# Optimization experiments

Measured on AMD Instinct MI355X. Metric: run time of the kernel, lower is better.

## Reference

```python
import jax, jax.numpy as jnp
import numpy as np

N = 50000      # nodes
DEG = 16       # avg random degree (self-loops added on top)
IN = 256       # in_dim
HID = 32       # num_hidden per head
H = 4          # heads for hidden layers
C = 64         # num_classes (output layer has 1 head of size C)
STEPS = 10     # label_prop_steps
SLOPE = 0.2    # negative_slope


def _glorot(k, shape):
    fan = shape[0] + int(np.prod(shape[1:]))
    return jax.random.normal(k, shape, jnp.float32) * np.sqrt(2.0 / fan)


def setup_inputs() -> dict:
    key = jax.random.key(0)
    ks = jax.random.split(key, 14)
    E0 = N * DEG
    loop = jnp.arange(N, dtype=jnp.int32)
    src = jnp.concatenate([jax.random.randint(ks[0], (E0,), 0, N, jnp.int32), loop])
    dst = jnp.concatenate([jax.random.randint(ks[1], (E0,), 0, N, jnp.int32), loop])
    feat = jax.random.normal(ks[2], (N, IN), jnp.float32)
    return {
        "feat": feat, "src": src, "dst": dst,
        # layer 0: in=256 -> [4 heads, 32]
        "W0": _glorot(ks[3], (IN, H, HID)), "al0": _glorot(ks[4], (H, HID)), "ar0": _glorot(ks[5], (H, HID)),
        # layer 1: in=128 -> [4 heads, 32]
        "W1": _glorot(ks[6], (H * HID, H, HID)), "al1": _glorot(ks[7], (H, HID)), "ar1": _glorot(ks[8], (H, HID)),
        # output layer: in=128 -> [1 head, 64]
        "W2": _glorot(ks[9], (H * HID, 1, C)), "al2": _glorot(ks[10], (1, C)), "ar2": _glorot(ks[11], (1, C)),
        # weighted-pooling layer (num_classes -> num_classes, no activation)
        "Wp": _glorot(ks[12], (C, C)), "bp": jnp.zeros((C,), jnp.float32),
    }


def gat_layer(x, src, dst, W, al, ar):
    """GAT conv: returns (out [N,H,D], alpha [E,H])."""
    n = x.shape[0]
    h = jnp.einsum('ni,ihd->nhd', x, W)                    # [N,H,D]
    el = jnp.sum(h * al, axis=-1)                          # [N,H]
    er = jnp.sum(h * ar, axis=-1)                          # [N,H]
    e = el[src] + er[dst]                                  # [E,H]
    e = jnp.where(e > 0, e, SLOPE * e)                     # LeakyReLU
    m = jax.ops.segment_max(e, dst, num_segments=n)        # edge softmax over incoming edges
    p = jnp.exp(e - m[dst])
    s = jax.ops.segment_sum(p, dst, num_segments=n)
    alpha = p / (s[dst] + 1e-9)                            # [E,H]
    out = jax.ops.segment_sum(h[src] * alpha[:, :, None], dst, num_segments=n)
    return out, alpha


def reference(feat, src, dst, W0, al0, ar0, W1, al1, ar1, W2, al2, ar2, Wp, bp):
    # GAT trunk: hidden layers flatten heads + ELU, output layer means heads.
    h, a0 = gat_layer(feat, src, dst, W0, al0, ar0)
    h = jax.nn.elu(h).reshape(N, H * HID)
    h, a1 = gat_layer(h, src, dst, W1, al1, ar1)
    h = jax.nn.elu(h).reshape(N, H * HID)
    out, a2 = gat_layer(h, src, dst, W2, al2, ar2)
    logits = out.mean(axis=1)                              # [N,C]

    # mean attention over heads per layer, then over layers; detached in original
    w = jax.lax.stop_gradient(
        (a0.mean(axis=1) + a1.mean(axis=1) + a2.mean(axis=1)) / 3.0)  # [E]

    # iterative label propagation via weighted pooling + linear (num_classes->num_classes)
    pseudo = jax.nn.softmax(logits, axis=1)
    for _ in range(STEPS):
        agg = jax.ops.segment_sum(w[:, None] * pseudo[src], dst, num_segments=N)  # [N,C]
        logits = agg @ Wp + bp
        pseudo = jax.nn.softmax(logits, axis=1)
    return jnp.log(pseudo)
```

## Files before the change

kernel.cpp:

```cpp
#include <hip/hip_runtime.h>
#include <math.h>

typedef _Float16 half_t;
typedef __attribute__((ext_vector_type(2))) _Float16 half2t;
typedef __attribute__((ext_vector_type(8))) _Float16 half8;
typedef __attribute__((ext_vector_type(4))) float f32x4;

__device__ __forceinline__ half2t u2h2(unsigned u){ half2t h; __builtin_memcpy(&h, &u, 4); return h; }
__device__ __forceinline__ unsigned h22u(half2t h){ unsigned u; __builtin_memcpy(&u, &h, 4); return u; }
__device__ __forceinline__ unsigned packh2(float a, float b){
  half2t h; h[0] = (_Float16)a; h[1] = (_Float16)b; return h22u(h);
}

__device__ __forceinline__ float wsumf(float v){
#pragma unroll
  for (int off = 1; off < 64; off <<= 1) v += __shfl_xor(v, off, 64);
  return v;
}


__global__ void k_zerob(int* __restrict__ a, int n){
  int i = blockIdx.x * blockDim.x + threadIdx.x;
  if (i < n) a[i] = 0;
}

__global__ __launch_bounds__(256) void kb_hist(
    const int* __restrict__ dst, int* __restrict__ bsum, int E, int NB)
{
  __shared__ int cnt[512];
  int t = threadIdx.x;
  int e00 = blockIdx.x * 2048;
  for (int i = t; i < NB; i += 256) cnt[i] = 0;
  __syncthreads();
#pragma unroll
  for (int k = 0; k < 8; k++){
    int e = e00 + 256 * k + t;
    if (e < E) atomicAdd(&cnt[dst[e] >> 7], 1);
  }
  __syncthreads();
  for (int i = t; i < NB; i += 256){
    int c = cnt[i];
    if (c) atomicAdd(&bsum[i], c);
  }
}

__global__ __launch_bounds__(512) void kb_scan(
    const int* __restrict__ bsum, int* __restrict__ bb, int* __restrict__ gcur,
    int E, int NB)
{
  __shared__ int sh[512];
  int t = threadIdx.x;
  int v = (t < NB) ? bsum[t] : 0;
  sh[t] = v; __syncthreads();
  for (int s = 1; s < 512; s <<= 1){
    int u = (t >= s) ? sh[t - s] : 0;
    __syncthreads();
    sh[t] += u;
    __syncthreads();
  }
  if (t < NB){
    int ex = sh[t] - v;
    bb[t] = ex; gcur[t] = ex;
  }
  if (t == 0) bb[NB] = E;
}

__global__ __launch_bounds__(256) void kb_scat(
    const int* __restrict__ src, const int* __restrict__ dst,
    int* __restrict__ gcur, int2* __restrict__ ebuf, int E, int NB)
{
  __shared__ int cnt[512], base[512];
  int t = threadIdx.x;
  int e00 = blockIdx.x * 2048;
  for (int i = t; i < NB; i += 256) cnt[i] = 0;
  __syncthreads();
  int bk[8], sv[8], dv[8];
#pragma unroll
  for (int k = 0; k < 8; k++){
    int e = e00 + 256 * k + t;
    if (e < E){
      dv[k] = dst[e]; sv[k] = src[e];
      bk[k] = dv[k] >> 7;
      atomicAdd(&cnt[bk[k]], 1);
    } else bk[k] = -1;
  }
  __syncthreads();
  for (int i = t; i < NB; i += 256){
    int c = cnt[i];
    base[i] = c ? atomicAdd(&gcur[i], c) : 0;
    cnt[i] = 0;
  }
  __syncthreads();
#pragma unroll
  for (int k = 0; k < 8; k++){
    if (bk[k] >= 0){
      int pos = base[bk[k]] + atomicAdd(&cnt[bk[k]], 1);
      ebuf[pos] = make_int2(sv[k], dv[k]);
    }
  }
}

__global__ __launch_bounds__(256) void kb_sort(
    const int2* __restrict__ ebuf, const int* __restrict__ bb,
    int* __restrict__ ptre, int* __restrict__ srcs, int N, int E)
{
  __shared__ int cnt[128], off[128];
  int b = blockIdx.x, t = threadIdx.x;
  int e0 = bb[b], e1 = bb[b + 1];
  int nn0 = b << 7;
  if (t < 128) cnt[t] = 0;
  __syncthreads();
  for (int e = e0 + t; e < e1; e += 256)
    atomicAdd(&cnt[ebuf[e].y & 127], 1);
  __syncthreads();
  if (t < 128) off[t] = cnt[t];
  __syncthreads();
  for (int s = 1; s < 128; s <<= 1){
    int v = (t < 128 && t >= s) ? off[t - s] : 0;
    __syncthreads();
    if (t < 128) off[t] += v;
    __syncthreads();
  }
  if (t < 128){
    int ex = off[t] - cnt[t];
    off[t] = ex;
    int node = nn0 + t;
    if (node < N) ptre[node] = e0 + ex;
    cnt[t] = 0;
  }
  if (b == (int)gridDim.x - 1 && t == 0) ptre[N] = E;
  __syncthreads();
  for (int e = e0 + t; e < e1; e += 256){
    int2 ed = ebuf[e];
    int lo = ed.y & 127;
    int pos = atomicAdd(&cnt[lo], 1);
    srcs[e0 + off[lo] + pos] = ed.x;
  }
}

__global__ void k_cvtw(const float* __restrict__ W0, const float* __restrict__ W1,
                       const float* __restrict__ W2, const float* __restrict__ Wp,
                       half_t* __restrict__ T0, half_t* __restrict__ T1,
                       half_t* __restrict__ T2, half_t* __restrict__ Tp){
  int i = blockIdx.x * 256 + threadIdx.x;
  const float* src; half_t* dst; int NN, KK, idx;
  if (i < 32768){ src = W0; dst = T0; NN = 128; KK = 256; idx = i; }
  else if (i < 49152){ src = W1; dst = T1; NN = 128; KK = 128; idx = i - 32768; }
  else if (i < 57344){ src = W2; dst = T2; NN = 64; KK = 128; idx = i - 49152; }
  else { src = Wp; dst = Tp; NN = 64; KK = 64; idx = i - 57344; }
  int nn = idx / KK, kk = idx - nn * KK;
  dst[idx] = (_Float16)src[(size_t)kk * NN + nn];
}

template<int NC, int NH, bool XF32>
__global__ __launch_bounds__(256) void k_gemm_m(
    const void* __restrict__ Xv, const half_t* __restrict__ Wt,
    const float* __restrict__ al, const float* __restrict__ ar,
    half_t* __restrict__ Yh, float* __restrict__ el, float* __restrict__ er,
    int n, int KD)
{
  constexpr int CT = NC / 16;
  __shared__ __align__(16) half_t xs[64 * 72];
  __shared__ __align__(16) half_t ws[NC * 72];
  int tid = threadIdx.x;
  int w = tid >> 6, lane = tid & 63;
  int m = lane & 15, q = lane >> 4;
  int n0 = blockIdx.x * 64;
  f32x4 acc[CT];
#pragma unroll
  for (int ct = 0; ct < CT; ct++) acc[ct] = (f32x4){0.f, 0.f, 0.f, 0.f};

  for (int kc = 0; kc < KD; kc += 64){
    if (XF32){
      const float* X = (const float*)Xv;
#pragma unroll
      for (int s = tid; s < 512; s += 256){
        int r = s >> 3, off = (s & 7) * 8;
        int gr = min(n0 + r, n - 1);
        const float4* g = (const float4*)(X + (size_t)gr * KD + kc + off);
        float4 v0 = g[0], v1 = g[1];
        uint4 pk = make_uint4(packh2(v0.x, v0.y), packh2(v0.z, v0.w),
                              packh2(v1.x, v1.y), packh2(v1.z, v1.w));
        *(uint4*)&xs[r * 72 + off] = pk;
      }
    } else {
      const half_t* X = (const half_t*)Xv;
#pragma unroll
      for (int s = tid; s < 512; s += 256){
        int r = s >> 3, off = (s & 7) * 8;
        int gr = min(n0 + r, n - 1);
        *(uint4*)&xs[r * 72 + off] = *(const uint4*)(X + (size_t)gr * KD + kc + off);
      }
    }
#pragma unroll
    for (int s = tid; s < NC * 8; s += 256){
      int r = s >> 3, off = (s & 7) * 8;
      *(uint4*)&ws[r * 72 + off] = *(const uint4*)(Wt + (size_t)r * KD + kc + off);
    }
    __syncthreads();
    half8 a0 = *(const half8*)&xs[(16 * w + m) * 72 + q * 8];
    half8 a1 = *(const half8*)&xs[(16 * w + m) * 72 + 32 + q * 8];
#pragma unroll
    for (int ct = 0; ct < CT; ct++){
      half8 b0 = *(const half8*)&ws[(16 * ct + m) * 72 + q * 8];
      half8 b1 = *(const half8*)&ws[(16 * ct + m) * 72 + 32 + q * 8];
      acc[ct] = __builtin_amdgcn_mfma_f32_16x16x32_f16(a0, b0, acc[ct], 0, 0, 0);
      acc[ct] = __builtin_amdgcn_mfma_f32_16x16x32_f16(a1, b1, acc[ct], 0, 0, 0);
    }
    __syncthreads();
  }

#pragma unroll
  for (int j = 0; j < 4; j++){
    int gr = n0 + 16 * w + q * 4 + j;
    if (gr < n){
#pragma unroll
      for (int ct = 0; ct < CT; ct++)
        Yh[(size_t)gr * NC + 16 * ct + m] = (_Float16)acc[ct][j];
    }
  }
  float alv[CT], arv[CT];
#pragma unroll
  for (int ct = 0; ct < CT; ct++){ alv[ct] = al[16 * ct + m]; arv[ct] = ar[16 * ct + m]; }
#pragma unroll
  for (int j = 0; j < 4; j++){
    int gr = n0 + 16 * w + q * 4 + j;
    float ev[NH], rv[NH];
    if (NH == 4){
#pragma unroll
      for (int hh = 0; hh < 4; hh++){
        ev[hh] = acc[2 * hh][j] * alv[2 * hh] + acc[2 * hh + 1][j] * alv[2 * hh + 1];
        rv[hh] = acc[2 * hh][j] * arv[2 * hh] + acc[2 * hh + 1][j] * arv[2 * hh + 1];
      }
    } else {
      ev[0] = 0.f; rv[0] = 0.f;
#pragma unroll
      for (int ct = 0; ct < CT; ct++){
        ev[0] += acc[ct][j] * alv[ct];
        rv[0] += acc[ct][j] * arv[ct];
      }
    }
#pragma unroll
    for (int off = 1; off < 16; off <<= 1){
#pragma unroll
      for (int hh = 0; hh < NH; hh++){
        ev[hh] += __shfl_xor(ev[hh], off, 64);
        rv[hh] += __shfl_xor(rv[hh], off, 64);
      }
    }
    if (m == 0 && gr < n){
#pragma unroll
      for (int hh = 0; hh < NH; hh++){
        el[(size_t)gr * NH + hh] = ev[hh];
        er[(size_t)gr * NH + hh] = rv[hh];
      }
    }
  }
}

template<int HNUM, int MDIM, int EPI>
__global__ __launch_bounds__(64) void k_edge(
    const int* __restrict__ ptre, const int* __restrict__ srcs,
    const char* __restrict__ hb, const float* __restrict__ el,
    const float* __restrict__ er, half_t* __restrict__ outx,
    unsigned char* __restrict__ outu, float* __restrict__ wE,
    int2* __restrict__ epk, int init_w, int n)
{
  constexpr int LL = MDIM / 8;
  constexpr int EP = 64 / LL;
  constexpr int RB = MDIM * 2;
  constexpr int HID = MDIM / HNUM;
  __shared__ unsigned au[HNUM][264];
  __shared__ int sids[256];
  int node = blockIdx.x;
  if (node >= n) return;
  int lane = threadIdx.x;
  int base = ptre[node], deg = ptre[node + 1] - base;

  float erv[HNUM];
  if (HNUM == 4){
    float4 t = *reinterpret_cast<const float4*>(er + node * 4);
    erv[0] = t.x; erv[1] = t.y; erv[2] = t.z; erv[3] = t.w;
  } else erv[0] = er[node];

  int l = lane % LL, g = lane / LL;
  int hidx = (8 * l) / HID;
  half2t acc2[4];
#pragma unroll
  for (int k = 0; k < 4; k++) acc2[k] = (half2t){(_Float16)0.f, (_Float16)0.f};

  if (deg <= 64){
    float pv[HNUM], sm[HNUM];
#pragma unroll
    for (int h = 0; h < HNUM; h++){ pv[h] = 0.f; sm[h] = 0.f; }
    int s = -1;
    if (lane < deg){
      s = srcs[base + lane];
      sids[lane] = s * RB;
      float e[HNUM];
      if (HNUM == 4){
        float4 t = *reinterpret_cast<const float4*>(el + s * 4);
        e[0] = t.x; e[1] = t.y; e[2] = t.z; e[3] = t.w;
      } else e[0] = el[s];
#pragma unroll
      for (int h = 0; h < HNUM; h++){
        float v = e[h] + erv[h];
        v = v > 0.f ? v : 0.2f * v;
        pv[h] = __expf(v);
        sm[h] = pv[h];
      }
    }
    float inv[HNUM];
#pragma unroll
    for (int h = 0; h < HNUM; h++) inv[h] = 1.f / (wsumf(sm[h]) + 1e-9f);
    if (lane < deg){
      float wsum = 0.f;
#pragma unroll
      for (int h = 0; h < HNUM; h++){
        float a = pv[h] * inv[h];
        wsum += a;
        au[h][lane] = packh2(a, a);
      }
      wsum *= (1.f / (3.f * HNUM));
      int eidx = base + lane;
      if (EPI == 1){
        float wtot = (wE[eidx] + wsum) * (1.f / 255.f);
        epk[eidx] = make_int2(s * 64, __float_as_int(wtot));
      } else {
        wE[eidx] = init_w ? wsum : (wE[eidx] + wsum);
      }
    }
    __syncthreads();
    for (int j0 = 0; j0 < deg; j0 += EP){
      int j = j0 + g;
      if (j < deg){
        half2t a2 = u2h2(au[hidx][j]);
        uint4 v = *(const uint4*)(hb + (unsigned)sids[j] + 16 * l);
        acc2[0] += a2 * u2h2(v.x);
        acc2[1] += a2 * u2h2(v.y);
        acc2[2] += a2 * u2h2(v.z);
        acc2[3] += a2 * u2h2(v.w);
      }
    }
  } else {
    float sm[HNUM];
#pragma unroll
    for (int h = 0; h < HNUM; h++) sm[h] = 0.f;
    for (int i = lane; i < deg; i += 64){
      int s = srcs[base + i];
      if (i < 256) sids[i] = s * RB;
      float e[HNUM];
      if (HNUM == 4){
        float4 t = *reinterpret_cast<const float4*>(el + s * 4);
        e[0] = t.x; e[1] = t.y; e[2] = t.z; e[3] = t.w;
      } else e[0] = el[s];
#pragma unroll
      for (int h = 0; h < HNUM; h++){
        float v = e[h] + erv[h];
        v = v > 0.f ? v : 0.2f * v;
        float p = __expf(v);
        sm[h] += p;
        if (i < 256) au[h][i] = __float_as_uint(p);
      }
    }
    float inv[HNUM];
#pragma unroll
    for (int h = 0; h < HNUM; h++) inv[h] = 1.f / (wsumf(sm[h]) + 1e-9f);

    for (int c0 = 0; c0 < deg; c0 += 256){
      int cnt = min(256, deg - c0);
      for (int i = lane; i < cnt; i += 64){
        float p[HNUM]; int soff;
        if (c0 == 0){
          soff = sids[i];
#pragma unroll
          for (int h = 0; h < HNUM; h++) p[h] = __uint_as_float(au[h][i]);
        } else {
          int s = srcs[base + c0 + i];
          soff = s * RB;
          sids[i] = soff;
          float e[HNUM];
          if (HNUM == 4){
            float4 t = *reinterpret_cast<const float4*>(el + s * 4);
            e[0] = t.x; e[1] = t.y; e[2] = t.z; e[3] = t.w;
          } else e[0] = el[s];
#pragma unroll
          for (int h = 0; h < HNUM; h++){
            float v = e[h] + erv[h];
            v = v > 0.f ? v : 0.2f * v;
            p[h] = __expf(v);
          }
        }
        float wsum = 0.f;
#pragma unroll
        for (int h = 0; h < HNUM; h++){
          float a = p[h] * inv[h];
          wsum += a;
          au[h][i] = packh2(a, a);
        }
        wsum *= (1.f / (3.f * HNUM));
        int eidx = base + c0 + i;
        if (EPI == 1){
          float wtot = (wE[eidx] + wsum) * (1.f / 255.f);
          epk[eidx] = make_int2(soff >> 1, __float_as_int(wtot));
        } else {
          wE[eidx] = init_w ? wsum : (wE[eidx] + wsum);
        }
      }
      __syncthreads();
      for (int j0 = 0; j0 < cnt; j0 += EP){
        int j = j0 + g;
        if (j < cnt){
          half2t a2 = u2h2(au[hidx][j]);
          uint4 v = *(const uint4*)(hb + (unsigned)sids[j] + 16 * l);
          acc2[0] += a2 * u2h2(v.x);
          acc2[1] += a2 * u2h2(v.y);
          acc2[2] += a2 * u2h2(v.z);
          acc2[3] += a2 * u2h2(v.w);
        }
      }
      __syncthreads();
    }
  }

#pragma unroll
  for (int off = LL; off < 64; off <<= 1)
#pragma unroll
    for (int k = 0; k < 4; k++)
      acc2[k] += u2h2((unsigned)__shfl_xor((int)h22u(acc2[k]), off, 64));

  float o[8];
#pragma unroll
  for (int k = 0; k < 4; k++){
    o[2 * k] = (float)acc2[k][0];
    o[2 * k + 1] = (float)acc2[k][1];
  }
  if (EPI == 0){
    if (g == 0){
#pragma unroll
      for (int d = 0; d < 8; d++) o[d] = o[d] > 0.f ? o[d] : expm1f(o[d]);
      uint4 pk = make_uint4(packh2(o[0], o[1]), packh2(o[2], o[3]),
                            packh2(o[4], o[5]), packh2(o[6], o[7]));
      reinterpret_cast<uint4*>(outx + (size_t)node * MDIM)[l] = pk;
    }
  } else {
    float m8 = o[0];
#pragma unroll
    for (int d = 1; d < 8; d++) m8 = fmaxf(m8, o[d]);
#pragma unroll
    for (int off = 1; off < 8; off <<= 1) m8 = fmaxf(m8, __shfl_xor(m8, off, 64));
    float p[8], s8 = 0.f;
#pragma unroll
    for (int d = 0; d < 8; d++){ p[d] = __expf(o[d] - m8); s8 += p[d]; }
#pragma unroll
    for (int off = 1; off < 8; off <<= 1) s8 += __shfl_xor(s8, off, 64);
    float is = 255.f / s8;
    if (g == 0){
      unsigned b0 = 0, b1 = 0;
#pragma unroll
      for (int d = 0; d < 4; d++) b0 |= ((unsigned)(int)(p[d] * is + 0.5f)) << (8 * d);
#pragma unroll
      for (int d = 0; d < 4; d++) b1 |= ((unsigned)(int)(p[4 + d] * is + 0.5f)) << (8 * d);
      *reinterpret_cast<uint2*>(outu + (size_t)node * 64 + 8 * l) = make_uint2(b0, b1);
    }
  }
}

template<int FINAL>
__global__ __launch_bounds__(256) void k_lpu(
    const int* __restrict__ ptre, const int2* __restrict__ epk,
    const unsigned char* __restrict__ pb, const half_t* __restrict__ Tp,
    const float* __restrict__ bp, unsigned char* __restrict__ outu,
    float* __restrict__ outf, int n)
{
  __shared__ __align__(16) half_t xs[64 * 72];
  __shared__ __align__(16) half_t ws[64 * 72];
  __shared__ float bsh[64];
  int tid = threadIdx.x;
  int w = tid >> 6, lane = tid & 63;
  int n0 = blockIdx.x * 64;
#pragma unroll
  for (int s = tid; s < 512; s += 256){
    int r = s >> 3, off = (s & 7) * 8;
    *(uint4*)&ws[r * 72 + off] = *(const uint4*)(Tp + r * 64 + off);
  }
  if (tid < 64) bsh[tid] = bp[tid];

  int grp = tid >> 2;
  int l4 = tid & 3;
  int node = n0 + grp;
  float acc[16];
#pragma unroll
  for (int c = 0; c < 16; c++) acc[c] = 0.f;

  auto accum = [&](uint4 v, float wv){
#pragma unroll
    for (int b = 0; b < 4; b++){
      unsigned u = (&v.x)[b];
      acc[4 * b + 0] += wv * (float)(u & 0xffu);
      acc[4 * b + 1] += wv * (float)((u >> 8) & 0xffu);
      acc[4 * b + 2] += wv * (float)((u >> 16) & 0xffu);
      acc[4 * b + 3] += wv * (float)((u >> 24) & 0xffu);
    }
  };

  if (node < n){
    int j = ptre[node], endd = ptre[node + 1];
    int bo = 16 * l4;
    while (j + 4 <= endd){
      int2 e0 = epk[j], e1 = epk[j + 1], e2 = epk[j + 2], e3 = epk[j + 3];
      uint4 v0 = *(const uint4*)(pb + (unsigned)e0.x + bo);
      uint4 v1 = *(const uint4*)(pb + (unsigned)e1.x + bo);
      uint4 v2 = *(const uint4*)(pb + (unsigned)e2.x + bo);
      uint4 v3 = *(const uint4*)(pb + (unsigned)e3.x + bo);
      accum(v0, __int_as_float(e0.y));
      accum(v1, __int_as_float(e1.y));
      accum(v2, __int_as_float(e2.y));
      accum(v3, __int_as_float(e3.y));
      j += 4;
    }
    while (j < endd){
      int2 ep = epk[j];
      uint4 v = *(const uint4*)(pb + (unsigned)ep.x + bo);
      accum(v, __int_as_float(ep.y));
      j++;
    }
  }
  {
    half2t hp[8];
#pragma unroll
    for (int c = 0; c < 8; c++){
      hp[c][0] = (_Float16)acc[2 * c]; hp[c][1] = (_Float16)acc[2 * c + 1];
    }
    *(uint4*)&xs[grp * 72 + 16 * l4]     = *(uint4*)&hp[0];
    *(uint4*)&xs[grp * 72 + 16 * l4 + 8] = *(uint4*)&hp[4];
  }
  __syncthreads();

  int m = lane & 15, q = lane >> 4;
  f32x4 macc[4];
#pragma unroll
  for (int ct = 0; ct < 4; ct++) macc[ct] = (f32x4){0.f, 0.f, 0.f, 0.f};
  half8 a0 = *(const half8*)&xs[(16 * w + m) * 72 + q * 8];
  half8 a1 = *(const half8*)&xs[(16 * w + m) * 72 + 32 + q * 8];
#pragma unroll
  for (int ct = 0; ct < 4; ct++){
    half8 b0 = *(const half8*)&ws[(16 * ct + m) * 72 + q * 8];
    half8 b1 = *(const half8*)&ws[(16 * ct + m) * 72 + 32 + q * 8];
    macc[ct] = __builtin_amdgcn_mfma_f32_16x16x32_f16(a0, b0, macc[ct], 0, 0, 0);
    macc[ct] = __builtin_amdgcn_mfma_f32_16x16x32_f16(a1, b1, macc[ct], 0, 0, 0);
  }

#pragma unroll
  for (int j = 0; j < 4; j++){
    int gr = n0 + 16 * w + q * 4 + j;
    float v[4]; float mx = -INFINITY;
#pragma unroll
    for (int ct = 0; ct < 4; ct++){
      v[ct] = macc[ct][j] + bsh[16 * ct + m];
      mx = fmaxf(mx, v[ct]);
    }
#pragma unroll
    for (int off = 1; off < 16; off <<= 1) mx = fmaxf(mx, __shfl_xor(mx, off, 64));
    float p[4], s = 0.f;
#pragma unroll
    for (int ct = 0; ct < 4; ct++){ p[ct] = __expf(v[ct] - mx); s += p[ct]; }
#pragma unroll
    for (int off = 1; off < 16; off <<= 1) s += __shfl_xor(s, off, 64);
    if (gr < n){
      if (FINAL){
        float ls = __logf(s);
#pragma unroll
        for (int ct = 0; ct < 4; ct++)
          outf[(size_t)gr * 64 + 16 * ct + m] = v[ct] - mx - ls;
      } else {
        float is = 255.f / s;
#pragma unroll
        for (int ct = 0; ct < 4; ct++)
          outu[(size_t)gr * 64 + 16 * ct + m] =
              (unsigned char)(int)(p[ct] * is + 0.5f);
      }
    }
  }
}

extern "C" void kernel_launch(void* const* d_in, const int* in_sizes, int n_in,
                              void* d_out, int out_size, void* d_ws, size_t ws_size,
                              hipStream_t stream) {
  const float* feat = (const float*)d_in[0];
  const int*   src  = (const int*)d_in[1];
  const int*   dst  = (const int*)d_in[2];
  const float* W0   = (const float*)d_in[3];
  const float* al0  = (const float*)d_in[4];
  const float* ar0  = (const float*)d_in[5];
  const float* W1   = (const float*)d_in[6];
  const float* al1  = (const float*)d_in[7];
  const float* ar1  = (const float*)d_in[8];
  const float* W2   = (const float*)d_in[9];
  const float* al2  = (const float*)d_in[10];
  const float* ar2  = (const float*)d_in[11];
  const float* Wp   = (const float*)d_in[12];
  const float* bp   = (const float*)d_in[13];
  float* out = (float*)d_out;

  const int N = in_sizes[0] / 256;
  const int E = in_sizes[1];
  const int NB = (N + 127) / 128;

  char* p = (char*)d_ws;
  auto carve = [&](size_t bytes) -> void* {
    void* r = (void*)p;
    p += (bytes + 255) & ~(size_t)255;
    return r;
  };
  int*   ptr_i = (int*)carve((size_t)(N + 1) * 4);
  int*   bsum  = (int*)carve((size_t)NB * 4);
  int*   bb    = (int*)carve((size_t)(NB + 1) * 4);
  int*   gcur  = (int*)carve((size_t)NB * 4);
  int*   srcs  = (int*)carve((size_t)E * 4);
  float* wE    = (float*)carve((size_t)E * 4);
  int2*  epk   = (int2*)carve((size_t)E * 8);
  half_t* hb   = (half_t*)carve((size_t)N * 128 * 2);
  half_t* xb   = (half_t*)carve((size_t)N * 128 * 2);
  float* el    = (float*)carve((size_t)N * 4 * 4);
  float* er    = (float*)carve((size_t)N * 4 * 4);
  unsigned char* pbA = (unsigned char*)carve((size_t)N * 64);
  unsigned char* pbB = (unsigned char*)carve((size_t)N * 64);
  half_t* T0   = (half_t*)carve(32768 * 2);
  half_t* T1   = (half_t*)carve(16384 * 2);
  half_t* T2   = (half_t*)carve(8192 * 2);
  half_t* Tp   = (half_t*)carve(4096 * 2);
  int2* ebuf = epk;
  (void)ws_size; (void)n_in; (void)out_size;

  const int EB = (E + 2047) / 2048;
  k_zerob<<<(NB + 255) / 256, 256, 0, stream>>>(bsum, NB);
  kb_hist<<<EB, 256, 0, stream>>>(dst, bsum, E, NB);
  kb_scan<<<1, 512, 0, stream>>>(bsum, bb, gcur, E, NB);
  kb_scat<<<EB, 256, 0, stream>>>(src, dst, gcur, ebuf, E, NB);
  kb_sort<<<NB, 256, 0, stream>>>(ebuf, bb, ptr_i, srcs, N, E);
  k_cvtw<<<240, 256, 0, stream>>>(W0, W1, W2, Wp, T0, T1, T2, Tp);

  const int GG = (N + 63) / 64;
  k_gemm_m<128, 4, true><<<GG, 256, 0, stream>>>(feat, T0, al0, ar0, hb, el, er, N, 256);
  k_edge<4, 128, 0><<<N, 64, 0, stream>>>(ptr_i, srcs, (const char*)hb, el, er,
                                          xb, nullptr, wE, nullptr, 1, N);
  k_gemm_m<128, 4, false><<<GG, 256, 0, stream>>>(xb, T1, al1, ar1, hb, el, er, N, 128);
  k_edge<4, 128, 0><<<N, 64, 0, stream>>>(ptr_i, srcs, (const char*)hb, el, er,
                                          xb, nullptr, wE, nullptr, 0, N);
  k_gemm_m<64, 1, false><<<GG, 256, 0, stream>>>(xb, T2, al2, ar2, hb, el, er, N, 128);
  k_edge<1, 64, 1><<<N, 64, 0, stream>>>(ptr_i, srcs, (const char*)hb, el, er,
                                         nullptr, pbA, wE, epk, 0, N);

  unsigned char* cur = pbA; unsigned char* nxt = pbB;
  for (int st = 0; st < 10; st++){
    if (st == 9)
      k_lpu<1><<<GG, 256, 0, stream>>>(ptr_i, epk, cur, Tp, bp, nullptr, out, N);
    else
      k_lpu<0><<<GG, 256, 0, stream>>>(ptr_i, epk, cur, Tp, bp, nxt, nullptr, N);
    unsigned char* t = cur; cur = nxt; nxt = t;
  }
}
```

Measured before the change: 480.6 us.

## Pack four nodes per edge block via shuffles; split label-prop edges across two lanes

The edge-attention kernel now runs four nodes per 256-thread block, one wavefront each. Source offsets and attention weights are broadcast with wavefront shuffles instead of shared memory and block barriers, and high-degree nodes recompute exponentials per 64-edge chunk. The label-propagation kernel doubles its threads to 512 so each node's edge list is split between two lane groups, which are then combined with a shuffle before the MFMA step. The aim is less launch overhead, fewer syncs and more memory-level parallelism on the gathers, at the cost of recomputing exponentials for large degrees and leaving half the waves idle during the matmul.

```diff
diff --git a/kernel.cpp b/kernel.cpp
--- a/kernel.cpp
+++ b/kernel.cpp
@@ -17,7 +17,6 @@
   for (int off = 1; off < 64; off <<= 1) v += __shfl_xor(v, off, 64);
   return v;
 }
-
 
 __global__ void k_zerob(int* __restrict__ a, int n){
   int i = blockIdx.x * blockDim.x + threadIdx.x;
@@ -259,7 +258,7 @@
 }
 
 template<int HNUM, int MDIM, int EPI>
-__global__ __launch_bounds__(64) void k_edge(
+__global__ __launch_bounds__(256) void k_edge(
     const int* __restrict__ ptre, const int* __restrict__ srcs,
     const char* __restrict__ hb, const float* __restrict__ el,
     const float* __restrict__ er, half_t* __restrict__ outx,
@@ -269,12 +268,9 @@
   constexpr int LL = MDIM / 8;
   constexpr int EP = 64 / LL;
   constexpr int RB = MDIM * 2;
-  constexpr int HID = MDIM / HNUM;
-  __shared__ unsigned au[HNUM][264];
-  __shared__ int sids[256];
-  int node = blockIdx.x;
+  int node = blockIdx.x * 4 + (threadIdx.x >> 6);
   if (node >= n) return;
-  int lane = threadIdx.x;
+  int lane = threadIdx.x & 63;
   int base = ptre[node], deg = ptre[node + 1] - base;
 
   float erv[HNUM];
@@ -284,19 +280,19 @@
   } else erv[0] = er[node];
 
   int l = lane % LL, g = lane / LL;
-  int hidx = (8 * l) / HID;
+  int hidx = l >> 2;
+  int bo = 16 * l;
   half2t acc2[4];
 #pragma unroll
   for (int k = 0; k < 4; k++) acc2[k] = (half2t){(_Float16)0.f, (_Float16)0.f};
 
-  if (deg <= 64){
-    float pv[HNUM], sm[HNUM];
-#pragma unroll
-    for (int h = 0; h < HNUM; h++){ pv[h] = 0.f; sm[h] = 0.f; }
-    int s = -1;
-    if (lane < deg){
-      s = srcs[base + lane];
-      sids[lane] = s * RB;
+  float inv[HNUM];
+  if (deg > 64){
+    float sm[HNUM];
+#pragma unroll
+    for (int h = 0; h < HNUM; h++) sm[h] = 0.f;
+    for (int i = lane; i < deg; i += 64){
+      int s = srcs[base + i];
       float e[HNUM];
       if (HNUM == 4){
         float4 t = *reinterpret_cast<const float4*>(el + s * 4);
@@ -306,121 +302,76 @@
       for (int h = 0; h < HNUM; h++){
         float v = e[h] + erv[h];
         v = v > 0.f ? v : 0.2f * v;
+        sm[h] += __expf(v);
+      }
+    }
+#pragma unroll
+    for (int h = 0; h < HNUM; h++) inv[h] = 1.f / (wsumf(sm[h]) + 1e-9f);
+  }
+
+  for (int c0 = 0; c0 < deg; c0 += 64){
+    int cnt = min(64, deg - c0);
+    int soff = 0; unsigned pa = 0, pb2 = 0;
+    float pv[HNUM];
+    int s = 0;
+    if (lane < cnt){
+      s = srcs[base + c0 + lane];
+      float e[HNUM];
+      if (HNUM == 4){
+        float4 t = *reinterpret_cast<const float4*>(el + s * 4);
+        e[0] = t.x; e[1] = t.y; e[2] = t.z; e[3] = t.w;
+      } else e[0] = el[s];
+#pragma unroll
+      for (int h = 0; h < HNUM; h++){
+        float v = e[h] + erv[h];
+        v = v > 0.f ? v : 0.2f * v;
         pv[h] = __expf(v);
-        sm[h] = pv[h];
-      }
-    }
-    float inv[HNUM];
-#pragma unroll
-    for (int h = 0; h < HNUM; h++) inv[h] = 1.f / (wsumf(sm[h]) + 1e-9f);
-    if (lane < deg){
-      float wsum = 0.f;
-#pragma unroll
-      for (int h = 0; h < HNUM; h++){
-        float a = pv[h] * inv[h];
-        wsum += a;
-        au[h][lane] = packh2(a, a);
-      }
+      }
+    } else {
+#pragma unroll
+      for (int h = 0; h < HNUM; h++) pv[h] = 0.f;
+    }
+    if (deg <= 64){
+#pragma unroll
+      for (int h = 0; h < HNUM; h++) inv[h] = 1.f / (wsumf(pv[h]) + 1e-9f);
+    }
+    if (lane < cnt){
+      float a[HNUM], wsum = 0.f;
+#pragma unroll
+      for (int h = 0; h < HNUM; h++){ a[h] = pv[h] * inv[h]; wsum += a[h]; }
+      if (HNUM == 4){ pa = packh2(a[0], a[1]); pb2 = packh2(a[2], a[3]); }
+      else pa = packh2(a[0], a[0]);
       wsum *= (1.f / (3.f * HNUM));
-      int eidx = base + lane;
+      int eidx = base + c0 + lane;
       if (EPI == 1){
         float wtot = (wE[eidx] + wsum) * (1.f / 255.f);
         epk[eidx] = make_int2(s * 64, __float_as_int(wtot));
       } else {
         wE[eidx] = init_w ? wsum : (wE[eidx] + wsum);
       }
-    }
-    __syncthreads();
-    for (int j0 = 0; j0 < deg; j0 += EP){
+      soff = s * RB;
+    }
+    for (int j0 = 0; j0 < cnt; j0 += EP){
       int j = j0 + g;
-      if (j < deg){
-        half2t a2 = u2h2(au[hidx][j]);
-        uint4 v = *(const uint4*)(hb + (unsigned)sids[j] + 16 * l);
+      int so = __shfl(soff, j, 64);
+      unsigned paj = (unsigned)__shfl((int)pa, j, 64);
+      unsigned pbj = 0;
+      if (HNUM == 4) pbj = (unsigned)__shfl((int)pb2, j, 64);
+      if (j < cnt){
+        unsigned a2u;
+        if (HNUM == 4){
+          unsigned sel = (hidx < 2) ? paj : pbj;
+          unsigned hb16 = (hidx & 1) ? (sel >> 16) : (sel & 0xffffu);
+          a2u = hb16 | (hb16 << 16);
+        } else a2u = paj;
+        half2t a2 = u2h2(a2u);
+        uint4 v = *(const uint4*)(hb + (unsigned)so + bo);
         acc2[0] += a2 * u2h2(v.x);
         acc2[1] += a2 * u2h2(v.y);
         acc2[2] += a2 * u2h2(v.z);
         acc2[3] += a2 * u2h2(v.w);
       }
     }
-  } else {
-    float sm[HNUM];
-#pragma unroll
-    for (int h = 0; h < HNUM; h++) sm[h] = 0.f;
-    for (int i = lane; i < deg; i += 64){
-      int s = srcs[base + i];
-      if (i < 256) sids[i] = s * RB;
-      float e[HNUM];
-      if (HNUM == 4){
-        float4 t = *reinterpret_cast<const float4*>(el + s * 4);
-        e[0] = t.x; e[1] = t.y; e[2] = t.z; e[3] = t.w;
-      } else e[0] = el[s];
-#pragma unroll
-      for (int h = 0; h < HNUM; h++){
-        float v = e[h] + erv[h];
-        v = v > 0.f ? v : 0.2f * v;
-        float p = __expf(v);
-        sm[h] += p;
-        if (i < 256) au[h][i] = __float_as_uint(p);
-      }
-    }
-    float inv[HNUM];
-#pragma unroll
-    for (int h = 0; h < HNUM; h++) inv[h] = 1.f / (wsumf(sm[h]) + 1e-9f);
-
-    for (int c0 = 0; c0 < deg; c0 += 256){
-      int cnt = min(256, deg - c0);
-      for (int i = lane; i < cnt; i += 64){
-        float p[HNUM]; int soff;
-        if (c0 == 0){
-          soff = sids[i];
-#pragma unroll
-          for (int h = 0; h < HNUM; h++) p[h] = __uint_as_float(au[h][i]);
-        } else {
-          int s = srcs[base + c0 + i];
-          soff = s * RB;
-          sids[i] = soff;
-          float e[HNUM];
-          if (HNUM == 4){
-            float4 t = *reinterpret_cast<const float4*>(el + s * 4);
-            e[0] = t.x; e[1] = t.y; e[2] = t.z; e[3] = t.w;
-          } else e[0] = el[s];
-#pragma unroll
-          for (int h = 0; h < HNUM; h++){
-            float v = e[h] + erv[h];
-            v = v > 0.f ? v : 0.2f * v;
-            p[h] = __expf(v);
-          }
-        }
-        float wsum = 0.f;
-#pragma unroll
-        for (int h = 0; h < HNUM; h++){
-          float a = p[h] * inv[h];
-          wsum += a;
-          au[h][i] = packh2(a, a);
-        }
-        wsum *= (1.f / (3.f * HNUM));
-        int eidx = base + c0 + i;
-        if (EPI == 1){
-          float wtot = (wE[eidx] + wsum) * (1.f / 255.f);
-          epk[eidx] = make_int2(soff >> 1, __float_as_int(wtot));
-        } else {
-          wE[eidx] = init_w ? wsum : (wE[eidx] + wsum);
-        }
-      }
-      __syncthreads();
-      for (int j0 = 0; j0 < cnt; j0 += EP){
-        int j = j0 + g;
-        if (j < cnt){
-          half2t a2 = u2h2(au[hidx][j]);
-          uint4 v = *(const uint4*)(hb + (unsigned)sids[j] + 16 * l);
-          acc2[0] += a2 * u2h2(v.x);
-          acc2[1] += a2 * u2h2(v.y);
-          acc2[2] += a2 * u2h2(v.z);
-          acc2[3] += a2 * u2h2(v.w);
-        }
-      }
-      __syncthreads();
-    }
   }
 
 #pragma unroll
@@ -467,7 +418,7 @@
 }
 
 template<int FINAL>
-__global__ __launch_bounds__(256) void k_lpu(
+__global__ __launch_bounds__(512) void k_lpu(
     const int* __restrict__ ptre, const int2* __restrict__ epk,
     const unsigned char* __restrict__ pb, const half_t* __restrict__ Tp,
     const float* __restrict__ bp, unsigned char* __restrict__ outu,
@@ -479,15 +430,16 @@
   int tid = threadIdx.x;
   int w = tid >> 6, lane = tid & 63;
   int n0 = blockIdx.x * 64;
-#pragma unroll
-  for (int s = tid; s < 512; s += 256){
-    int r = s >> 3, off = (s & 7) * 8;
+  {
+    int r = tid >> 3, off = (tid & 7) * 8;
     *(uint4*)&ws[r * 72 + off] = *(const uint4*)(Tp + r * 64 + off);
   }
   if (tid < 64) bsh[tid] = bp[tid];
 
-  int grp = tid >> 2;
-  int l4 = tid & 3;
+  int grp = tid >> 3;
+  int l8 = tid & 7;
+  int st = l8 >> 2, li = l8 & 3;
+  int bo = 16 * li;
   int node = n0 + grp;
   float acc[16];
 #pragma unroll
@@ -505,37 +457,36 @@
   };
 
   if (node < n){
-    int j = ptre[node], endd = ptre[node + 1];
-    int bo = 16 * l4;
-    while (j + 4 <= endd){
-      int2 e0 = epk[j], e1 = epk[j + 1], e2 = epk[j + 2], e3 = epk[j + 3];
-      uint4 v0 = *(const uint4*)(pb + (unsigned)e0.x + bo);
-      uint4 v1 = *(const uint4*)(pb + (unsigned)e1.x + bo);
-      uint4 v2 = *(const uint4*)(pb + (unsigned)e2.x + bo);
-      uint4 v3 = *(const uint4*)(pb + (unsigned)e3.x + bo);
-      accum(v0, __int_as_float(e0.y));
-      accum(v1, __int_as_float(e1.y));
-      accum(v2, __int_as_float(e2.y));
-      accum(v3, __int_as_float(e3.y));
-      j += 4;
-    }
-    while (j < endd){
-      int2 ep = epk[j];
-      uint4 v = *(const uint4*)(pb + (unsigned)ep.x + bo);
-      accum(v, __int_as_float(ep.y));
-      j++;
-    }
-  }
-  {
+    int base = ptre[node], endd = ptre[node + 1];
+    for (int j0 = base + 4 * st; j0 < endd; j0 += 8){
+      int2 ee[4]; float wv[4];
+#pragma unroll
+      for (int k = 0; k < 4; k++){
+        int j = j0 + k;
+        ee[k] = epk[min(j, endd - 1)];
+        wv[k] = (j < endd) ? __int_as_float(ee[k].y) : 0.f;
+      }
+      uint4 vv[4];
+#pragma unroll
+      for (int k = 0; k < 4; k++)
+        vv[k] = *(const uint4*)(pb + (unsigned)ee[k].x + bo);
+#pragma unroll
+      for (int k = 0; k < 4; k++) accum(vv[k], wv[k]);
+    }
+  }
+#pragma unroll
+  for (int c = 0; c < 16; c++) acc[c] += __shfl_xor(acc[c], 4, 64);
+  if (st == 0){
     half2t hp[8];
 #pragma unroll
     for (int c = 0; c < 8; c++){
       hp[c][0] = (_Float16)acc[2 * c]; hp[c][1] = (_Float16)acc[2 * c + 1];
     }
-    *(uint4*)&xs[grp * 72 + 16 * l4]     = *(uint4*)&hp[0];
-    *(uint4*)&xs[grp * 72 + 16 * l4 + 8] = *(uint4*)&hp[4];
-  }
-  __syncthreads();
+    *(uint4*)&xs[grp * 72 + 16 * li]     = *(uint4*)&hp[0];
+    *(uint4*)&xs[grp * 72 + 16 * li + 8] = *(uint4*)&hp[4];
+  }
+  __syncthreads();
+  if (w >= 4) return;
 
   int m = lane & 15, q = lane >> 4;
   f32x4 macc[4];
@@ -642,22 +593,23 @@
   k_cvtw<<<240, 256, 0, stream>>>(W0, W1, W2, Wp, T0, T1, T2, Tp);
 
   const int GG = (N + 63) / 64;
+  const int GE = (N + 3) / 4;
   k_gemm_m<128, 4, true><<<GG, 256, 0, stream>>>(feat, T0, al0, ar0, hb, el, er, N, 256);
-  k_edge<4, 128, 0><<<N, 64, 0, stream>>>(ptr_i, srcs, (const char*)hb, el, er,
-                                          xb, nullptr, wE, nullptr, 1, N);
+  k_edge<4, 128, 0><<<GE, 256, 0, stream>>>(ptr_i, srcs, (const char*)hb, el, er,
+                                            xb, nullptr, wE, nullptr, 1, N);
   k_gemm_m<128, 4, false><<<GG, 256, 0, stream>>>(xb, T1, al1, ar1, hb, el, er, N, 128);
-  k_edge<4, 128, 0><<<N, 64, 0, stream>>>(ptr_i, srcs, (const char*)hb, el, er,
-                                          xb, nullptr, wE, nullptr, 0, N);
+  k_edge<4, 128, 0><<<GE, 256, 0, stream>>>(ptr_i, srcs, (const char*)hb, el, er,
+                                            xb, nullptr, wE, nullptr, 0, N);
   k_gemm_m<64, 1, false><<<GG, 256, 0, stream>>>(xb, T2, al2, ar2, hb, el, er, N, 128);
-  k_edge<1, 64, 1><<<N, 64, 0, stream>>>(ptr_i, srcs, (const char*)hb, el, er,
-                                         nullptr, pbA, wE, epk, 0, N);
+  k_edge<1, 64, 1><<<GE, 256, 0, stream>>>(ptr_i, srcs, (const char*)hb, el, er,
+                                           nullptr, pbA, wE, epk, 0, N);
 
   unsigned char* cur = pbA; unsigned char* nxt = pbB;
   for (int st = 0; st < 10; st++){
     if (st == 9)
-      k_lpu<1><<<GG, 256, 0, stream>>>(ptr_i, epk, cur, Tp, bp, nullptr, out, N);
+      k_lpu<1><<<GG, 512, 0, stream>>>(ptr_i, epk, cur, Tp, bp, nullptr, out, N);
     else
-      k_lpu<0><<<GG, 256, 0, stream>>>(ptr_i, epk, cur, Tp, bp, nxt, nullptr, N);
+      k_lpu<0><<<GG, 512, 0, stream>>>(ptr_i, epk, cur, Tp, bp, nxt, nullptr, N);
     unsigned char* t = cur; cur = nxt; nxt = t;
   }
 }
```

After: 475.2 us. No clear change (-1.1%).
